# Performance work log

Hardware: AMD Instinct MI355X
Metric: run time of the kernel (lower is better)

The kernel has to match this reference:

```python
import jax, jax.numpy as jnp
import numpy as np

D_MODEL, D_STATE, D_CONV, D_INNER = 1024, 16, 4, 2048
BATCH, SEQ = 2, 2048


def setup_inputs() -> dict:
    key = jax.random.key(0)
    ks = jax.random.split(key, 12)
    s = 0.02
    inp = {
        "x": jax.random.normal(ks[0], (BATCH, SEQ, D_MODEL), jnp.float32),
        # Linear weights stored (in, out): y = x @ W + b (equivalent to torch x @ W.T + b)
        "W_in": jax.random.normal(ks[1], (D_MODEL, 2 * D_INNER), jnp.float32) * s,
        "b_in": jnp.zeros((2 * D_INNER,), jnp.float32),
        # depthwise conv kernel (OIH) with groups=d_inner -> (d_inner, 1, d_conv)
        "conv_w": jax.random.normal(ks[2], (D_INNER, 1, D_CONV), jnp.float32) * s,
        "conv_b": jnp.zeros((D_INNER,), jnp.float32),
        "W_x": jax.random.normal(ks[3], (D_INNER, 2 * D_STATE), jnp.float32) * s,
        "b_x": jnp.zeros((2 * D_STATE,), jnp.float32),
        "W_dt": jax.random.normal(ks[4], (D_INNER, D_INNER), jnp.float32) * s,
        "b_dt": jnp.zeros((D_INNER,), jnp.float32),
        # A_log init: log(arange(1..d_state)) tiled over d_inner, as in the module
        "A_log": jnp.log(jnp.tile(jnp.arange(1, D_STATE + 1, dtype=jnp.float32), (D_INNER, 1))),
        "D": jnp.ones((D_INNER,), jnp.float32),
        "W_out": jax.random.normal(ks[5], (D_INNER, D_MODEL), jnp.float32) * s,
        "b_out": jnp.zeros((D_MODEL,), jnp.float32),
    }
    return inp


def reference(x, W_in, b_in, conv_w, conv_b, W_x, b_x, W_dt, b_dt, A_log, D, W_out, b_out):
    d_inner, d_state = A_log.shape
    d_conv = conv_w.shape[-1]
    bsz, seq_len, _ = x.shape

    xz = x @ W_in + b_in                      # (B, L, 2*Din)
    xh, z = jnp.split(xz, 2, axis=-1)

    # causal depthwise conv: torch pads both sides by d_conv-1 then slices [:L]
    # == left-pad-only causal conv
    xc = jnp.transpose(xh, (0, 2, 1))         # (B, Din, L)
    xc = jax.lax.conv_general_dilated(
        xc, conv_w, window_strides=(1,), padding=[(d_conv - 1, 0)],
        dimension_numbers=("NCH", "OIH", "NCH"), feature_group_count=d_inner)
    xc = xc + conv_b[None, :, None]
    xh = jax.nn.silu(jnp.transpose(xc, (0, 2, 1)))  # (B, L, Din)

    A = -jnp.exp(A_log)                       # (Din, N)
    x_dbl = xh @ W_x + b_x                    # (B, L, 2N)
    Bmat = x_dbl[..., d_state:]               # second chunk; first chunk is discarded
    delta = jax.nn.softplus(xh @ W_dt + b_dt) # (B, L, Din)

    def step(h, inp):
        d_t, b_t, u_t = inp                    # (B,Din), (B,N), (B,Din)
        dA = jnp.exp(d_t[:, :, None] * A)      # (B, Din, N)
        dBu = d_t[:, :, None] * b_t[:, None, :] * u_t[:, :, None]
        h = dA * h + dBu
        return h, h.sum(-1)                    # y_t: (B, Din)

    h0 = jnp.zeros((bsz, d_inner, d_state), x.dtype)
    _, ys = jax.lax.scan(step, h0, (jnp.swapaxes(delta, 0, 1),
                                    jnp.swapaxes(Bmat, 0, 1),
                                    jnp.swapaxes(xh, 0, 1)))
    y = jnp.swapaxes(ys, 0, 1) + xh * D       # skip connection with D
    y = y * jax.nn.silu(z)                    # gate
    return y @ W_out + b_out                  # (B, L, d_model)
```

## Files before the change

### kernel.cpp

```cpp
#include <hip/hip_runtime.h>
#include <stdint.h>

#define NDM   1024
#define NDS   16
#define NDC   4
#define NDI   2048
#define NB    2
#define NL    2048
#define MROWS (NB*NL)
#define CCH   32
#define CLEN  64

typedef __bf16 bf16x8 __attribute__((ext_vector_type(8)));
typedef float  f32x4  __attribute__((ext_vector_type(4)));
typedef short  short8 __attribute__((ext_vector_type(8)));

__device__ __forceinline__ short f2bf(float f) {
  union { float f; unsigned u; } x; x.f = f;
  unsigned r = (x.u + 0x7FFFu + ((x.u >> 16) & 1u)) >> 16;
  return (short)r;
}
__device__ __forceinline__ float bf2f(short s) {
  union { unsigned u; float f; } x; x.u = ((unsigned)(unsigned short)s) << 16;
  return x.f;
}

__device__ __forceinline__ size_t fgoff(int row, int k8, int K) {
  return (size_t)(row >> 4) * K * 16 + (size_t)k8 * 128 + (row & 15) * 8;
}

__global__ __launch_bounds__(256) void cvt_fg_kernel(
    const float* __restrict__ in, short* __restrict__ out) {
  __shared__ short slab[16][1032];
  const int tid = threadIdx.x;
  const int g = blockIdx.x;
  const float* p = in + (size_t)g * 16 * 1024;
  #pragma unroll
  for (int u = 0; u < 8; ++u) {
    int unit = u * 256 + tid;
    int rr = unit >> 7, cc = unit & 127;
    const float* rp = p + (size_t)rr * 1024 + cc * 8;
    #pragma unroll
    for (int e = 0; e < 8; ++e) slab[rr][cc * 8 + e] = f2bf(rp[e]);
  }
  __syncthreads();
  short* op = out + (size_t)g * 16384;
  #pragma unroll
  for (int u = 0; u < 8; ++u) {
    int u2 = u * 256 + tid;
    int rr = u2 & 15, k8 = u2 >> 4;
    *(short8*)&op[k8 * 128 + rr * 8] = *(short8*)&slab[rr][k8 * 8];
  }
}

__global__ __launch_bounds__(256) void transpose_fg_kernel(
    const float* __restrict__ in, short* __restrict__ out, int K, int N) {
  __shared__ float t[64][33];
  const int tx = threadIdx.x, ty = threadIdx.y;
  const int n0 = blockIdx.x * 32, k0 = blockIdx.y * 64;
  #pragma unroll
  for (int i = 0; i < 64; i += 8)
    t[ty + i][tx] = in[(size_t)(k0 + ty + i) * N + n0 + tx];
  __syncthreads();
  const int n = n0 + tx, k8 = (k0 >> 3) + ty;
  short8 v;
  #pragma unroll
  for (int e = 0; e < 8; ++e) v[e] = f2bf(t[ty * 8 + e][tx]);
  *(short8*)&out[fgoff(n, k8, K)] = v;
}

__global__ __launch_bounds__(256) void wx_fg_kernel(
    const float* __restrict__ Wx, short* __restrict__ Wcat) {
  int t = blockIdx.x * 256 + threadIdx.x;
  int k8 = t >> 4, n = t & 15;
  short8 v;
  #pragma unroll
  for (int e = 0; e < 8; ++e)
    v[e] = f2bf(Wx[(size_t)(k8 * 8 + e) * (2 * NDS) + NDS + n]);
  *(short8*)&Wcat[(size_t)128 * 2048 * 16 + (size_t)k8 * 128 + n * 8] = v;
}

template<int BN, int EPI>
__global__ __launch_bounds__(256, 2) void gemm_fg_kernel(
    const short* __restrict__ A, const short* __restrict__ Bt,
    const float* __restrict__ bias, float* __restrict__ C,
    short* __restrict__ Cb, float* __restrict__ Bm,
    const float* __restrict__ bx, int M, int N, int K)
{
  const int tid  = threadIdx.x;
  const int lane = tid & 63;
  const int w    = tid >> 6;
  const int wM   = w >> 1;
  const int wN   = w & 1;
  const int g    = lane >> 4;
  const int r    = lane & 15;

  constexpr int FN = BN / 32;

  const int nx  = gridDim.x;
  const int nwg = nx * gridDim.y;
  const int bid = blockIdx.y * nx + blockIdx.x;
  const int swz = (bid & 7) * (nwg >> 3) + (bid >> 3);
  const int bm  = (swz / nx) * 128;
  const int bn  = (swz % nx) * BN;

  const short* pA[4];
  const short* pB[FN];
  #pragma unroll
  for (int m = 0; m < 4; ++m)
    pA[m] = A + (size_t)((bm >> 4) + wM * 4 + m) * K * 16 + lane * 8;
  #pragma unroll
  for (int n = 0; n < FN; ++n)
    pB[n] = Bt + (size_t)((bn >> 4) + wN * FN + n) * K * 16 + lane * 8;

  f32x4 acc[4][FN];
  #pragma unroll
  for (int m = 0; m < 4; ++m)
    #pragma unroll
    for (int n = 0; n < FN; ++n)
      acc[m][n] = (f32x4){0.f, 0.f, 0.f, 0.f};

  bf16x8 a0[4], b0[FN], a1[4], b1[FN];
  #pragma unroll
  for (int m = 0; m < 4; ++m) a0[m] = *(const bf16x8*)(pA[m]);
  #pragma unroll
  for (int n = 0; n < FN; ++n) b0[n] = *(const bf16x8*)(pB[n]);

  for (int kb = 0; kb < K; kb += 64) {
    if (kb + 32 < K) {
      #pragma unroll
      for (int m = 0; m < 4; ++m)
        a1[m] = *(const bf16x8*)(pA[m] + (size_t)(kb + 32) * 16);
      #pragma unroll
      for (int n = 0; n < FN; ++n)
        b1[n] = *(const bf16x8*)(pB[n] + (size_t)(kb + 32) * 16);
    }
    #pragma unroll
    for (int m = 0; m < 4; ++m)
      #pragma unroll
      for (int n = 0; n < FN; ++n)
        acc[m][n] = __builtin_amdgcn_mfma_f32_16x16x32_bf16(
            a0[m], b0[n], acc[m][n], 0, 0, 0);

    if (kb + 64 < K) {
      #pragma unroll
      for (int m = 0; m < 4; ++m)
        a0[m] = *(const bf16x8*)(pA[m] + (size_t)(kb + 64) * 16);
      #pragma unroll
      for (int n = 0; n < FN; ++n)
        b0[n] = *(const bf16x8*)(pB[n] + (size_t)(kb + 64) * 16);
    }
    #pragma unroll
    for (int m = 0; m < 4; ++m)
      #pragma unroll
      for (int n = 0; n < FN; ++n)
        acc[m][n] = __builtin_amdgcn_mfma_f32_16x16x32_bf16(
            a1[m], b1[n], acc[m][n], 0, 0, 0);
  }

  if constexpr (EPI == 2) {
    __shared__ short ctile[128][136];
    #pragma unroll
    for (int m = 0; m < 4; ++m) {
      const int rl0 = wM * 64 + m * 16 + g * 4;
      #pragma unroll
      for (int n = 0; n < FN; ++n) {
        const int cl = wN * (BN / 2) + n * 16 + r;
        const float bv = bias[bn + cl];
        #pragma unroll
        for (int e = 0; e < 4; ++e)
          ctile[rl0 + e][cl] = f2bf(acc[m][n][e] + bv);
      }
    }
    __syncthreads();
    #pragma unroll
    for (int it = 0; it < (128 * BN / 8) / 256; ++it) {
      int id = it * 256 + tid;
      int rowL = id / (BN / 8), c8 = id % (BN / 8);
      *(short8*)&Cb[(size_t)(bm + rowL) * N + bn + c8 * 8] =
          *(short8*)&ctile[rowL][c8 * 8];
    }
  } else {
    #pragma unroll
    for (int m = 0; m < 4; ++m) {
      const int row0 = bm + wM * 64 + m * 16 + g * 4;
      #pragma unroll
      for (int n = 0; n < FN; ++n) {
        const int colbase = bn + wN * (BN / 2) + n * 16;
        const int col = colbase + r;
        if (EPI == 0 || colbase < 2048) {
          const float bv = bias[col];
          #pragma unroll
          for (int e = 0; e < 4; ++e) {
            float v = acc[m][n][e] + bv;
            if (EPI == 1) v = (v > 15.f) ? v : log1pf(__expf(v));
            C[(size_t)(row0 + e) * N + col] = v;
          }
        } else if (EPI == 1 && colbase < 2064) {
          const float bv = bx[NDS + r];
          #pragma unroll
          for (int e = 0; e < 4; ++e)
            Bm[(size_t)(row0 + e) * NDS + r] = acc[m][n][e] + bv;
        }
      }
    }
  }
}

__global__ __launch_bounds__(256) void conv_silu_kernel(
    const short* __restrict__ xz, const float* __restrict__ cw,
    const float* __restrict__ cb, float* __restrict__ xh,
    short* __restrict__ xhbf) {
  __shared__ short slab[16][528];
  const int tid = threadIdx.x;
  const int c0 = blockIdx.x * 512;
  const int r0 = blockIdx.y * 16;
  const int b  = r0 >> 11;
  const int t0 = r0 & (NL - 1);
  const short* zbase = xz + ((size_t)b * NL) * (2 * NDI);

  #pragma unroll
  for (int u = 0; u < 4; ++u) {
    int unit = u * 256 + tid;
    int rr = unit >> 6, cc = unit & 63;
    int t = t0 + rr, c = c0 + cc * 8;
    float acc[8];
    #pragma unroll
    for (int e = 0; e < 8; ++e) acc[e] = cb[c + e];
    #pragma unroll
    for (int k = 0; k < NDC; ++k) {
      int tt = t - (NDC - 1) + k;
      if (tt >= 0) {
        short8 rv = *(const short8*)(zbase + (size_t)tt * (2 * NDI) + c);
        #pragma unroll
        for (int e = 0; e < 8; ++e)
          acc[e] += cw[(c + e) * NDC + k] * bf2f(rv[e]);
      }
    }
    float* xo = xh + (size_t)(r0 + rr) * NDI + c;
    #pragma unroll
    for (int e = 0; e < 8; ++e) {
      float s = acc[e] / (1.f + __expf(-acc[e]));
      xo[e] = s;
      slab[rr][cc * 8 + e] = f2bf(s);
    }
  }
  __syncthreads();
  short* op = xhbf + (size_t)(r0 >> 4) * NDI * 16 + (size_t)(c0 >> 3) * 128;
  #pragma unroll
  for (int u = 0; u < 4; ++u) {
    int u2 = u * 256 + tid;
    int rr = u2 & 15, q = u2 >> 4;
    *(short8*)&op[q * 128 + rr * 8] = *(short8*)&slab[rr][q * 8];
  }
}

__device__ __forceinline__ size_t scoff(int b, int k, int c) {
  return (((size_t)b * CCH + k) * NDI + c) * NDS;
}

__global__ __launch_bounds__(256) void scan_p1_kernel(
    const float* __restrict__ delta, const float* __restrict__ Bm,
    const float* __restrict__ xh, const float* __restrict__ A_log,
    float* __restrict__ Pbuf, float* __restrict__ Hend) {
  const int i = blockIdx.x * 256 + threadIdx.x;
  const int c = i & (NDI - 1);
  const int k = (i >> 11) & (CCH - 1);
  const int b = i >> 16;
  const int t0 = k * CLEN;

  float Av[NDS];
  #pragma unroll
  for (int s = 0; s < NDS; ++s) Av[s] = -__expf(A_log[c * NDS + s]);

  const float* dp = delta + ((size_t)(b * NL + t0)) * NDI + c;
  const float* up = xh    + ((size_t)(b * NL + t0)) * NDI + c;
  const f32x4* Bp = (const f32x4*)(Bm + ((size_t)(b * NL + t0)) * NDS);

  float h[NDS], P[NDS];
  #pragma unroll
  for (int s = 0; s < NDS; ++s) { h[s] = 0.f; P[s] = 1.f; }

  #pragma unroll 4
  for (int j = 0; j < CLEN; ++j) {
    const float d = dp[(size_t)j * NDI];
    const float u = up[(size_t)j * NDI];
    f32x4 B0 = Bp[j * 4 + 0], B1 = Bp[j * 4 + 1];
    f32x4 B2 = Bp[j * 4 + 2], B3 = Bp[j * 4 + 3];
    const float du = d * u;
    float Bv[NDS];
    #pragma unroll
    for (int e = 0; e < 4; ++e) {
      Bv[e] = B0[e]; Bv[4 + e] = B1[e]; Bv[8 + e] = B2[e]; Bv[12 + e] = B3[e];
    }
    #pragma unroll
    for (int s = 0; s < NDS; ++s) {
      float dA = __expf(d * Av[s]);
      h[s] = dA * h[s] + du * Bv[s];
      P[s] *= dA;
    }
  }

  const size_t base = scoff(b, k, c);
  #pragma unroll
  for (int q = 0; q < 4; ++q) {
    *(f32x4*)&Pbuf[base + q * 4] = (f32x4){P[q*4], P[q*4+1], P[q*4+2], P[q*4+3]};
    *(f32x4*)&Hend[base + q * 4] = (f32x4){h[q*4], h[q*4+1], h[q*4+2], h[q*4+3]};
  }
}

__global__ __launch_bounds__(256) void scan_p2_kernel(
    const float* __restrict__ Pbuf, const float* __restrict__ Hend,
    float* __restrict__ Hin) {
  const int i = blockIdx.x * 256 + threadIdx.x;
  const int s = i & (NDS - 1);
  const int c = (i >> 4) & (NDI - 1);
  const int b = i >> 15;
  const size_t step = (size_t)NDI * NDS;
  const size_t base = scoff(b, 0, c) + s;
  float h = 0.f;
  #pragma unroll 8
  for (int k = 0; k < CCH; ++k) {
    Hin[base + (size_t)k * step] = h;
    h = Hend[base + (size_t)k * step] + Pbuf[base + (size_t)k * step] * h;
  }
}

__global__ __launch_bounds__(256) void scan_p3_kernel(
    const float* __restrict__ delta, const float* __restrict__ Bm,
    const float* __restrict__ xh, const float* __restrict__ A_log,
    const float* __restrict__ Hin, const float* __restrict__ Dvec,
    const short* __restrict__ xz, short* __restrict__ ybf) {
  const int tid = threadIdx.x;
  const int i = blockIdx.x * 256 + tid;
  const int c = i & (NDI - 1);
  const int k = (i >> 11) & (CCH - 1);
  const int b = i >> 16;
  const int t0 = k * CLEN;
  const int cb0 = (blockIdx.x * 256) & (NDI - 1);

  __shared__ float ylds[16][257];

  float Av[NDS];
  #pragma unroll
  for (int s = 0; s < NDS; ++s) Av[s] = -__expf(A_log[c * NDS + s]);
  const float dcoef = Dvec[c];

  const float* dp = delta + ((size_t)(b * NL + t0)) * NDI + c;
  const float* up = xh    + ((size_t)(b * NL + t0)) * NDI + c;
  const f32x4* Bp = (const f32x4*)(Bm + ((size_t)(b * NL + t0)) * NDS);
  const short* zp = xz    + ((size_t)(b * NL + t0)) * (2 * NDI) + NDI + c;

  const size_t base = scoff(b, k, c);
  float h[NDS];
  #pragma unroll
  for (int s = 0; s < NDS; ++s) h[s] = Hin[base + s];

  for (int j = 0; j < CLEN; ++j) {
    const float d = dp[(size_t)j * NDI];
    const float u = up[(size_t)j * NDI];
    f32x4 B0 = Bp[j * 4 + 0], B1 = Bp[j * 4 + 1];
    f32x4 B2 = Bp[j * 4 + 2], B3 = Bp[j * 4 + 3];
    const float du = d * u;
    float Bv[NDS];
    #pragma unroll
    for (int e = 0; e < 4; ++e) {
      Bv[e] = B0[e]; Bv[4 + e] = B1[e]; Bv[8 + e] = B2[e]; Bv[12 + e] = B3[e];
    }
    #pragma unroll
    for (int s = 0; s < NDS; ++s) {
      float dA = __expf(d * Av[s]);
      h[s] = dA * h[s] + du * Bv[s];
    }
    float sum01 = 0.f, sum23 = 0.f;
    #pragma unroll
    for (int s = 0; s < 8; ++s)  sum01 += h[s];
    #pragma unroll
    for (int s = 8; s < 16; ++s) sum23 += h[s];
    float y = sum01 + sum23 + u * dcoef;
    float z = bf2f(zp[(size_t)j * (2 * NDI)]);
    y *= z / (1.f + __expf(-z));
    ylds[j & 15][tid] = y;

    if ((j & 15) == 15) {
      __syncthreads();
      const int jb = j - 15;
      #pragma unroll
      for (int s2 = 0; s2 < 2; ++s2) {
        int u2 = tid + 256 * s2;
        int tt = u2 & 15, q = u2 >> 4;
        short8 v;
        #pragma unroll
        for (int e = 0; e < 8; ++e) v[e] = f2bf(ylds[tt][q * 8 + e]);
        int grow = b * NL + t0 + jb + tt;
        int k8 = (cb0 >> 3) + q;
        *(short8*)&ybf[fgoff(grow, k8, NDI)] = v;
      }
      __syncthreads();
    }
  }
}

extern "C" void kernel_launch(void* const* d_in, const int* in_sizes, int n_in,
                              void* d_out, int out_size, void* d_ws, size_t ws_size,
                              hipStream_t stream) {
  const float* x      = (const float*)d_in[0];
  const float* W_in   = (const float*)d_in[1];
  const float* b_in   = (const float*)d_in[2];
  const float* conv_w = (const float*)d_in[3];
  const float* conv_b = (const float*)d_in[4];
  const float* W_x    = (const float*)d_in[5];
  const float* b_x    = (const float*)d_in[6];
  const float* W_dt   = (const float*)d_in[7];
  const float* b_dt   = (const float*)d_in[8];
  const float* A_log  = (const float*)d_in[9];
  const float* Dv     = (const float*)d_in[10];
  const float* W_out  = (const float*)d_in[11];
  const float* b_out  = (const float*)d_in[12];
  float* out = (float*)d_out;

  char* w = (char*)d_ws;
  short* xbf   = (short*)(w);
  short* WtIn  = (short*)(w + 8388608);
  short* WtCat = (short*)(w + 16777216);
  short* WtOut = (short*)(w + 25690112);
  short* xzbf  = (short*)(w + 29884416);
  float* xhf   = (float*)(w + 63438848);
  short* xhbf  = (short*)(w + 96993280);
  float* delta = (float*)(w + 113770496);
  float* Bm    = (float*)(w + 147324928);
  short* ybf   = (short*)(w + 147587072);
  float* Pbuf  = (float*)(w);
  float* Hend  = (float*)(w + 8388608);
  float* Hin   = (float*)(w + 16777216);

  hipMemsetAsync((char*)WtCat + (size_t)129 * 65536, 0, 7 * 65536, stream);

  cvt_fg_kernel<<<MROWS / 16, 256, 0, stream>>>(x, xbf);
  transpose_fg_kernel<<<dim3((2 * NDI) / 32, NDM / 64), dim3(32, 8), 0, stream>>>(
      W_in, WtIn, NDM, 2 * NDI);
  transpose_fg_kernel<<<dim3(NDI / 32, NDI / 64), dim3(32, 8), 0, stream>>>(
      W_dt, WtCat, NDI, NDI);
  wx_fg_kernel<<<16, 256, 0, stream>>>(W_x, WtCat);
  transpose_fg_kernel<<<dim3(NDM / 32, NDI / 64), dim3(32, 8), 0, stream>>>(
      W_out, WtOut, NDI, NDM);

  gemm_fg_kernel<128, 2><<<dim3((2 * NDI) / 128, MROWS / 128), 256, 0, stream>>>(
      xbf, WtIn, b_in, nullptr, xzbf, nullptr, nullptr,
      MROWS, 2 * NDI, NDM);

  conv_silu_kernel<<<dim3(NDI / 512, MROWS / 16), 256, 0, stream>>>(
      xzbf, conv_w, conv_b, xhf, xhbf);

  gemm_fg_kernel<128, 1><<<dim3(2176 / 128, MROWS / 128), 256, 0, stream>>>(
      xhbf, WtCat, b_dt, delta, nullptr, Bm, b_x,
      MROWS, NDI, NDI);

  scan_p1_kernel<<<(NB * NDI * CCH) / 256, 256, 0, stream>>>(
      delta, Bm, xhf, A_log, Pbuf, Hend);
  scan_p2_kernel<<<(NB * NDI * NDS) / 256, 256, 0, stream>>>(Pbuf, Hend, Hin);
  scan_p3_kernel<<<(NB * NDI * CCH) / 256, 256, 0, stream>>>(
      delta, Bm, xhf, A_log, Hin, Dv, xzbf, ybf);

  gemm_fg_kernel<64, 0><<<dim3(NDM / 64, MROWS / 128), 256, 0, stream>>>(
      ybf, WtOut, b_out, out, nullptr, nullptr, nullptr,
      MROWS, NDM, NDI);
}
```

Measured before the change: 327.4 us.

## Stage GEMM tiles in LDS via direct global-to-LDS loads with 256-row blocks

The bf16 MFMA GEMM moves from per-wave register loads straight from global memory to double-buffered LDS staging filled with global_load_lds DMA. It also grows blocks to 512 threads covering 256 output rows. Waves now share A and B tiles instead of each fetching its own operands, which cuts global traffic and raises data reuse per block. In exchange the grids are halved, so the last two GEMMs launch only a few hundred blocks. Correctness also depends on the barrier waiting for the asynchronous LDS loads to finish.

```diff
diff --git a/kernel.cpp b/kernel.cpp
--- a/kernel.cpp
+++ b/kernel.cpp
@@ -29,6 +29,13 @@
   return (size_t)(row >> 4) * K * 16 + (size_t)k8 * 128 + (row & 15) * 8;
 }
 
+__device__ __forceinline__ void gload16(const void* g, void* l) {
+  __builtin_amdgcn_global_load_lds(
+      (__attribute__((address_space(1))) void*)(uintptr_t)g,
+      (__attribute__((address_space(3))) void*)l,
+      16, 0, 0);
+}
+
 __global__ __launch_bounds__(256) void cvt_fg_kernel(
     const float* __restrict__ in, short* __restrict__ out) {
   __shared__ short slab[16][1032];
@@ -81,7 +88,7 @@
 }
 
 template<int BN, int EPI>
-__global__ __launch_bounds__(256, 2) void gemm_fg_kernel(
+__global__ __launch_bounds__(512, 2) void gemm_fg_kernel(
     const short* __restrict__ A, const short* __restrict__ Bt,
     const float* __restrict__ bias, float* __restrict__ C,
     short* __restrict__ Cb, float* __restrict__ Bm,
@@ -90,82 +97,88 @@
   const int tid  = threadIdx.x;
   const int lane = tid & 63;
   const int w    = tid >> 6;
-  const int wM   = w >> 1;
-  const int wN   = w & 1;
+  const int wM   = w >> 2;
+  const int wN   = w & 3;
   const int g    = lane >> 4;
   const int r    = lane & 15;
 
-  constexpr int FN = BN / 32;
+  constexpr int FNB  = BN / 64;
+  constexpr int NBG  = BN / 16;
+  constexpr int ABUF = 8192;
+  constexpr int BBUF = BN * 32;
+  constexpr int STG  = 2 * (ABUF + BBUF);
+  constexpr int POOL = (EPI == 2 && STG < 256 * 136) ? 256 * 136 : STG;
+  __shared__ short pool[POOL];
+#define BUFA(b) (pool + (b) * (ABUF + BBUF))
+#define BUFB(b) (pool + ABUF + (b) * (ABUF + BBUF))
 
   const int nx  = gridDim.x;
   const int nwg = nx * gridDim.y;
   const int bid = blockIdx.y * nx + blockIdx.x;
   const int swz = (bid & 7) * (nwg >> 3) + (bid >> 3);
-  const int bm  = (swz / nx) * 128;
+  const int bm  = (swz / nx) * 256;
   const int bn  = (swz % nx) * BN;
 
-  const short* pA[4];
-  const short* pB[FN];
-  #pragma unroll
-  for (int m = 0; m < 4; ++m)
-    pA[m] = A + (size_t)((bm >> 4) + wM * 4 + m) * K * 16 + lane * 8;
-  #pragma unroll
-  for (int n = 0; n < FN; ++n)
-    pB[n] = Bt + (size_t)((bn >> 4) + wN * FN + n) * K * 16 + lane * 8;
-
-  f32x4 acc[4][FN];
-  #pragma unroll
-  for (int m = 0; m < 4; ++m)
-    #pragma unroll
-    for (int n = 0; n < FN; ++n)
+  const short* pA[2];
+  #pragma unroll
+  for (int q = 0; q < 2; ++q)
+    pA[q] = A + (size_t)((bm >> 4) + 2 * w + q) * K * 16 + lane * 8;
+  const short* pB =
+      Bt + (size_t)((bn >> 4) + (w < NBG ? w : 0)) * K * 16 + lane * 8;
+
+#define STAGE(buf, kb)                                                   \
+  do {                                                                   \
+    _Pragma("unroll")                                                    \
+    for (int q = 0; q < 2; ++q)                                          \
+      gload16(pA[q] + (size_t)(kb) * 16, BUFA(buf) + (2 * w + q) * 512 + \
+              lane * 8 - lane * 8);                                      \
+    if (w < NBG)                                                         \
+      gload16(pB + (size_t)(kb) * 16, BUFB(buf) + w * 512);              \
+  } while (0)
+
+
+  f32x4 acc[8][FNB];
+  #pragma unroll
+  for (int m = 0; m < 8; ++m)
+    #pragma unroll
+    for (int n = 0; n < FNB; ++n)
       acc[m][n] = (f32x4){0.f, 0.f, 0.f, 0.f};
 
-  bf16x8 a0[4], b0[FN], a1[4], b1[FN];
-  #pragma unroll
-  for (int m = 0; m < 4; ++m) a0[m] = *(const bf16x8*)(pA[m]);
-  #pragma unroll
-  for (int n = 0; n < FN; ++n) b0[n] = *(const bf16x8*)(pB[n]);
-
-  for (int kb = 0; kb < K; kb += 64) {
-    if (kb + 32 < K) {
+  STAGE(0, 0);
+  int cur = 0;
+  for (int kb = 0; kb < K; kb += 32) {
+    __syncthreads();
+    if (kb + 32 < K) STAGE(cur ^ 1, kb + 32);
+
+    bf16x8 af[8], bfv[FNB];
+    #pragma unroll
+    for (int m = 0; m < 8; ++m)
+      af[m] = *(const bf16x8*)(BUFA(cur) + (wM * 8 + m) * 512 + lane * 8);
+    #pragma unroll
+    for (int n = 0; n < FNB; ++n)
+      bfv[n] = *(const bf16x8*)(BUFB(cur) + (wN * FNB + n) * 512 + lane * 8);
+
+    #pragma unroll
+    for (int m = 0; m < 8; ++m)
       #pragma unroll
-      for (int m = 0; m < 4; ++m)
-        a1[m] = *(const bf16x8*)(pA[m] + (size_t)(kb + 32) * 16);
+      for (int n = 0; n < FNB; ++n)
+        acc[m][n] = __builtin_amdgcn_mfma_f32_16x16x32_bf16(
+            af[m], bfv[n], acc[m][n], 0, 0, 0);
+    cur ^= 1;
+  }
+#undef STAGE
+#undef BUFA
+#undef BUFB
+
+  if constexpr (EPI == 2) {
+    __syncthreads();
+    short (*ctile)[136] = (short(*)[136])pool;
+    #pragma unroll
+    for (int m = 0; m < 8; ++m) {
+      const int rl0 = wM * 128 + m * 16 + g * 4;
       #pragma unroll
-      for (int n = 0; n < FN; ++n)
-        b1[n] = *(const bf16x8*)(pB[n] + (size_t)(kb + 32) * 16);
-    }
-    #pragma unroll
-    for (int m = 0; m < 4; ++m)
-      #pragma unroll
-      for (int n = 0; n < FN; ++n)
-        acc[m][n] = __builtin_amdgcn_mfma_f32_16x16x32_bf16(
-            a0[m], b0[n], acc[m][n], 0, 0, 0);
-
-    if (kb + 64 < K) {
-      #pragma unroll
-      for (int m = 0; m < 4; ++m)
-        a0[m] = *(const bf16x8*)(pA[m] + (size_t)(kb + 64) * 16);
-      #pragma unroll
-      for (int n = 0; n < FN; ++n)
-        b0[n] = *(const bf16x8*)(pB[n] + (size_t)(kb + 64) * 16);
-    }
-    #pragma unroll
-    for (int m = 0; m < 4; ++m)
-      #pragma unroll
-      for (int n = 0; n < FN; ++n)
-        acc[m][n] = __builtin_amdgcn_mfma_f32_16x16x32_bf16(
-            a1[m], b1[n], acc[m][n], 0, 0, 0);
-  }
-
-  if constexpr (EPI == 2) {
-    __shared__ short ctile[128][136];
-    #pragma unroll
-    for (int m = 0; m < 4; ++m) {
-      const int rl0 = wM * 64 + m * 16 + g * 4;
-      #pragma unroll
-      for (int n = 0; n < FN; ++n) {
-        const int cl = wN * (BN / 2) + n * 16 + r;
+      for (int n = 0; n < FNB; ++n) {
+        const int cl = wN * (BN / 4) + n * 16 + r;
         const float bv = bias[bn + cl];
         #pragma unroll
         for (int e = 0; e < 4; ++e)
@@ -173,20 +186,21 @@
       }
     }
     __syncthreads();
-    #pragma unroll
-    for (int it = 0; it < (128 * BN / 8) / 256; ++it) {
-      int id = it * 256 + tid;
-      int rowL = id / (BN / 8), c8 = id % (BN / 8);
+    constexpr int CPR = BN / 8;
+    #pragma unroll
+    for (int it = 0; it < (256 * CPR) / 512; ++it) {
+      int id = it * 512 + tid;
+      int rowL = id / CPR, c8 = id % CPR;
       *(short8*)&Cb[(size_t)(bm + rowL) * N + bn + c8 * 8] =
           *(short8*)&ctile[rowL][c8 * 8];
     }
   } else {
     #pragma unroll
-    for (int m = 0; m < 4; ++m) {
-      const int row0 = bm + wM * 64 + m * 16 + g * 4;
+    for (int m = 0; m < 8; ++m) {
+      const int row0 = bm + wM * 128 + m * 16 + g * 4;
       #pragma unroll
-      for (int n = 0; n < FN; ++n) {
-        const int colbase = bn + wN * (BN / 2) + n * 16;
+      for (int n = 0; n < FNB; ++n) {
+        const int colbase = bn + wN * (BN / 4) + n * 16;
         const int col = colbase + r;
         if (EPI == 0 || colbase < 2048) {
           const float bv = bias[col];
@@ -445,14 +459,14 @@
   transpose_fg_kernel<<<dim3(NDM / 32, NDI / 64), dim3(32, 8), 0, stream>>>(
       W_out, WtOut, NDI, NDM);
 
-  gemm_fg_kernel<128, 2><<<dim3((2 * NDI) / 128, MROWS / 128), 256, 0, stream>>>(
+  gemm_fg_kernel<128, 2><<<dim3((2 * NDI) / 128, MROWS / 256), 512, 0, stream>>>(
       xbf, WtIn, b_in, nullptr, xzbf, nullptr, nullptr,
       MROWS, 2 * NDI, NDM);
 
   conv_silu_kernel<<<dim3(NDI / 512, MROWS / 16), 256, 0, stream>>>(
       xzbf, conv_w, conv_b, xhf, xhbf);
 
-  gemm_fg_kernel<128, 1><<<dim3(2176 / 128, MROWS / 128), 256, 0, stream>>>(
+  gemm_fg_kernel<128, 1><<<dim3(2176 / 128, MROWS / 256), 512, 0, stream>>>(
       xhbf, WtCat, b_dt, delta, nullptr, Bm, b_x,
       MROWS, NDI, NDI);
 
@@ -462,7 +476,7 @@
   scan_p3_kernel<<<(NB * NDI * CCH) / 256, 256, 0, stream>>>(
       delta, Bm, xhf, A_log, Hin, Dv, xzbf, ybf);
 
-  gemm_fg_kernel<64, 0><<<dim3(NDM / 64, MROWS / 128), 256, 0, stream>>>(
+  gemm_fg_kernel<64, 0><<<dim3(NDM / 64, MROWS / 256), 512, 0, stream>>>(
       ybf, WtOut, b_out, out, nullptr, nullptr, nullptr,
       MROWS, NDM, NDI);
 }
```

Result: no change. 326.8 us (-0.2%).

## Store delta and conv output as bf16 in fragment layout for scan

Applied to the files above, without the earlier changes.

The conv kernel no longer writes an fp32 copy of the activated input. The delta GEMM epilogue now writes softplus output as bf16 through shared memory in the same 16-row fragment-grouped layout as xhbf. The scan kernels read both delta and u from these bf16 fragment-layout buffers, which roughly halves scan input traffic and removes two large fp32 writes. The cost is reduced precision in delta, which feeds an exp inside a long recurrence, plus strided 2-byte loads in the scan.

```diff
diff --git a/kernel.cpp b/kernel.cpp
--- a/kernel.cpp
+++ b/kernel.cpp
@@ -96,6 +96,7 @@
   const int r    = lane & 15;
 
   constexpr int FN = BN / 32;
+  __shared__ short ctile_s[(EPI == 0) ? 2 : 128 * 136];
 
   const int nx  = gridDim.x;
   const int nwg = nx * gridDim.y;
@@ -159,13 +160,13 @@
   }
 
   if constexpr (EPI == 2) {
-    __shared__ short ctile[128][136];
+    short (*ctile)[136] = (short(*)[136])ctile_s;
     #pragma unroll
     for (int m = 0; m < 4; ++m) {
       const int rl0 = wM * 64 + m * 16 + g * 4;
       #pragma unroll
       for (int n = 0; n < FN; ++n) {
-        const int cl = wN * (BN / 2) + n * 16 + r;
+        const int cl = wN * 64 + n * 16 + r;
         const float bv = bias[bn + cl];
         #pragma unroll
         for (int e = 0; e < 4; ++e)
@@ -180,23 +181,25 @@
       *(short8*)&Cb[(size_t)(bm + rowL) * N + bn + c8 * 8] =
           *(short8*)&ctile[rowL][c8 * 8];
     }
-  } else {
+  } else if constexpr (EPI == 1) {
+    short (*ctile)[136] = (short(*)[136])ctile_s;
     #pragma unroll
     for (int m = 0; m < 4; ++m) {
-      const int row0 = bm + wM * 64 + m * 16 + g * 4;
+      const int rl0 = wM * 64 + m * 16 + g * 4;
+      const int row0 = bm + rl0;
       #pragma unroll
       for (int n = 0; n < FN; ++n) {
-        const int colbase = bn + wN * (BN / 2) + n * 16;
-        const int col = colbase + r;
-        if (EPI == 0 || colbase < 2048) {
-          const float bv = bias[col];
+        const int colbase = bn + wN * 64 + n * 16;
+        if (colbase < 2048) {
+          const int cl = wN * 64 + n * 16 + r;
+          const float bv = bias[colbase + r];
           #pragma unroll
           for (int e = 0; e < 4; ++e) {
             float v = acc[m][n][e] + bv;
-            if (EPI == 1) v = (v > 15.f) ? v : log1pf(__expf(v));
-            C[(size_t)(row0 + e) * N + col] = v;
+            v = (v > 15.f) ? v : log1pf(__expf(v));
+            ctile[rl0 + e][cl] = f2bf(v);
           }
-        } else if (EPI == 1 && colbase < 2064) {
+        } else if (colbase == 2048) {
           const float bv = bx[NDS + r];
           #pragma unroll
           for (int e = 0; e < 4; ++e)
@@ -204,13 +207,37 @@
         }
       }
     }
+    __syncthreads();
+    if (bn < 2048) {
+      #pragma unroll
+      for (int it = 0; it < 8; ++it) {
+        int unit = it * 256 + tid;
+        int grp = unit >> 8, wi = unit & 255;
+        int k8l = wi >> 4, rr = wi & 15;
+        *(short8*)&Cb[(size_t)((bm >> 4) + grp) * (NDI * 16) +
+                      (size_t)((bn >> 3) + k8l) * 128 + rr * 8] =
+            *(short8*)&ctile[grp * 16 + rr][k8l * 8];
+      }
+    }
+  } else {
+    #pragma unroll
+    for (int m = 0; m < 4; ++m) {
+      const int row0 = bm + wM * 64 + m * 16 + g * 4;
+      #pragma unroll
+      for (int n = 0; n < FN; ++n) {
+        const int col = bn + wN * (BN / 2) + n * 16 + r;
+        const float bv = bias[col];
+        #pragma unroll
+        for (int e = 0; e < 4; ++e)
+          C[(size_t)(row0 + e) * N + col] = acc[m][n][e] + bv;
+      }
+    }
   }
 }
 
 __global__ __launch_bounds__(256) void conv_silu_kernel(
     const short* __restrict__ xz, const float* __restrict__ cw,
-    const float* __restrict__ cb, float* __restrict__ xh,
-    short* __restrict__ xhbf) {
+    const float* __restrict__ cb, short* __restrict__ xhbf) {
   __shared__ short slab[16][528];
   const int tid = threadIdx.x;
   const int c0 = blockIdx.x * 512;
@@ -237,11 +264,9 @@
           acc[e] += cw[(c + e) * NDC + k] * bf2f(rv[e]);
       }
     }
-    float* xo = xh + (size_t)(r0 + rr) * NDI + c;
     #pragma unroll
     for (int e = 0; e < 8; ++e) {
       float s = acc[e] / (1.f + __expf(-acc[e]));
-      xo[e] = s;
       slab[rr][cc * 8 + e] = f2bf(s);
     }
   }
@@ -260,8 +285,8 @@
 }
 
 __global__ __launch_bounds__(256) void scan_p1_kernel(
-    const float* __restrict__ delta, const float* __restrict__ Bm,
-    const float* __restrict__ xh, const float* __restrict__ A_log,
+    const short* __restrict__ dbf, const float* __restrict__ Bm,
+    const short* __restrict__ xhbf, const float* __restrict__ A_log,
     float* __restrict__ Pbuf, float* __restrict__ Hend) {
   const int i = blockIdx.x * 256 + threadIdx.x;
   const int c = i & (NDI - 1);
@@ -273,8 +298,10 @@
   #pragma unroll
   for (int s = 0; s < NDS; ++s) Av[s] = -__expf(A_log[c * NDS + s]);
 
-  const float* dp = delta + ((size_t)(b * NL + t0)) * NDI + c;
-  const float* up = xh    + ((size_t)(b * NL + t0)) * NDI + c;
+  const size_t fgb = (size_t)((b * NL + t0) >> 4) * (NDI * 16) +
+                     (size_t)(c >> 3) * 128 + (c & 7);
+  const short* up = xhbf + fgb;
+  const short* dp = dbf + fgb;
   const f32x4* Bp = (const f32x4*)(Bm + ((size_t)(b * NL + t0)) * NDS);
 
   float h[NDS], P[NDS];
@@ -283,8 +310,9 @@
 
   #pragma unroll 4
   for (int j = 0; j < CLEN; ++j) {
-    const float d = dp[(size_t)j * NDI];
-    const float u = up[(size_t)j * NDI];
+    const size_t o = (size_t)(j >> 4) * (NDI * 16) + (j & 15) * 8;
+    const float d = bf2f(dp[o]);
+    const float u = bf2f(up[o]);
     f32x4 B0 = Bp[j * 4 + 0], B1 = Bp[j * 4 + 1];
     f32x4 B2 = Bp[j * 4 + 2], B3 = Bp[j * 4 + 3];
     const float du = d * u;
@@ -327,8 +355,8 @@
 }
 
 __global__ __launch_bounds__(256) void scan_p3_kernel(
-    const float* __restrict__ delta, const float* __restrict__ Bm,
-    const float* __restrict__ xh, const float* __restrict__ A_log,
+    const short* __restrict__ dbf, const float* __restrict__ Bm,
+    const short* __restrict__ xhbf, const float* __restrict__ A_log,
     const float* __restrict__ Hin, const float* __restrict__ Dvec,
     const short* __restrict__ xz, short* __restrict__ ybf) {
   const int tid = threadIdx.x;
@@ -346,10 +374,12 @@
   for (int s = 0; s < NDS; ++s) Av[s] = -__expf(A_log[c * NDS + s]);
   const float dcoef = Dvec[c];
 
-  const float* dp = delta + ((size_t)(b * NL + t0)) * NDI + c;
-  const float* up = xh    + ((size_t)(b * NL + t0)) * NDI + c;
+  const size_t fgb = (size_t)((b * NL + t0) >> 4) * (NDI * 16) +
+                     (size_t)(c >> 3) * 128 + (c & 7);
+  const short* up = xhbf + fgb;
+  const short* dp = dbf + fgb;
   const f32x4* Bp = (const f32x4*)(Bm + ((size_t)(b * NL + t0)) * NDS);
-  const short* zp = xz    + ((size_t)(b * NL + t0)) * (2 * NDI) + NDI + c;
+  const short* zp = xz + ((size_t)(b * NL + t0)) * (2 * NDI) + NDI + c;
 
   const size_t base = scoff(b, k, c);
   float h[NDS];
@@ -357,8 +387,9 @@
   for (int s = 0; s < NDS; ++s) h[s] = Hin[base + s];
 
   for (int j = 0; j < CLEN; ++j) {
-    const float d = dp[(size_t)j * NDI];
-    const float u = up[(size_t)j * NDI];
+    const size_t o = (size_t)(j >> 4) * (NDI * 16) + (j & 15) * 8;
+    const float d = bf2f(dp[o]);
+    const float u = bf2f(up[o]);
     f32x4 B0 = Bp[j * 4 + 0], B1 = Bp[j * 4 + 1];
     f32x4 B2 = Bp[j * 4 + 2], B3 = Bp[j * 4 + 3];
     const float du = d * u;
@@ -425,9 +456,8 @@
   short* WtCat = (short*)(w + 16777216);
   short* WtOut = (short*)(w + 25690112);
   short* xzbf  = (short*)(w + 29884416);
-  float* xhf   = (float*)(w + 63438848);
   short* xhbf  = (short*)(w + 96993280);
-  float* delta = (float*)(w + 113770496);
+  short* dbf   = (short*)(w + 113770496);
   float* Bm    = (float*)(w + 147324928);
   short* ybf   = (short*)(w + 147587072);
   float* Pbuf  = (float*)(w);
@@ -450,17 +480,17 @@
       MROWS, 2 * NDI, NDM);
 
   conv_silu_kernel<<<dim3(NDI / 512, MROWS / 16), 256, 0, stream>>>(
-      xzbf, conv_w, conv_b, xhf, xhbf);
+      xzbf, conv_w, conv_b, xhbf);
 
   gemm_fg_kernel<128, 1><<<dim3(2176 / 128, MROWS / 128), 256, 0, stream>>>(
-      xhbf, WtCat, b_dt, delta, nullptr, Bm, b_x,
+      xhbf, WtCat, b_dt, nullptr, dbf, Bm, b_x,
       MROWS, NDI, NDI);
 
   scan_p1_kernel<<<(NB * NDI * CCH) / 256, 256, 0, stream>>>(
-      delta, Bm, xhf, A_log, Pbuf, Hend);
+      dbf, Bm, xhbf, A_log, Pbuf, Hend);
   scan_p2_kernel<<<(NB * NDI * NDS) / 256, 256, 0, stream>>>(Pbuf, Hend, Hin);
   scan_p3_kernel<<<(NB * NDI * CCH) / 256, 256, 0, stream>>>(
-      delta, Bm, xhf, A_log, Hin, Dv, xzbf, ybf);
+      dbf, Bm, xhbf, A_log, Hin, Dv, xzbf, ybf);
 
   gemm_fg_kernel<64, 0><<<dim3(NDM / 64, MROWS / 128), 256, 0, stream>>>(
       ybf, WtOut, b_out, out, nullptr, nullptr, nullptr,
```

Result: no change. 328.4 us (+0.3%).
